# Optimization experiments

Measured on AMD Instinct MI355X. Metric: run time of the kernel, lower is better.

Reference implementation:

```python
import jax, jax.numpy as jnp
import numpy as np

N_INT4, N_INT8, K, GROUP = 6144, 2048, 8192, 128
N_TOTAL = N_INT4 + N_INT8
M = 16


def setup_inputs() -> dict:
    key = jax.random.key(0)
    ks = jax.random.split(key, 8)
    x = jax.random.normal(ks[0], (M, K), jnp.float32)
    # uint4 weights: values 0..15 (stored int32)
    w_int4 = jax.random.randint(ks[1], (N_INT4, K), 0, 16, jnp.int32)
    # group-wise scales [N_int4, K//group_size]
    s_int4 = jax.random.uniform(ks[2], (N_INT4, K // GROUP), jnp.float32, minval=0.005, maxval=0.02)
    # int8 weights stored in offset-128 form (w_int8 + 128 -> 0..255), as pack_for_marlin builds
    w_uint8 = jax.random.randint(ks[3], (N_INT8, K), 0, 256, jnp.int32)
    # per-channel int8 scales
    s_int8 = jax.random.uniform(ks[4], (N_INT8,), jnp.float32, minval=0.005, maxval=0.02)
    awq_scales = jax.random.uniform(ks[5], (K,), jnp.float32, minval=0.5, maxval=2.0)
    bias = jax.random.normal(ks[6], (N_TOTAL,), jnp.float32) * 0.01
    inv_perm = jax.random.permutation(ks[7], N_TOTAL).astype(jnp.int32)
    return dict(x=x, w_int4=w_int4, s_int4=s_int4, w_uint8=w_uint8, s_int8=s_int8,
                awq_scales=awq_scales, bias=bias, inv_perm=inv_perm, group_size=GROUP)


def reference(x, w_int4, s_int4, w_uint8, s_int8, awq_scales, bias, inv_perm, group_size):
    dt = x.dtype
    k = x.shape[-1]
    # AWQ input scaling (unfused path: x / awq_scales)
    x2 = x.reshape(-1, k) / awq_scales[None, :]
    sum_x = jnp.sum(x2, axis=1, keepdims=True)  # [M, 1]

    # Marlin uint4b8 dequant: (q - 8) * scale, group-wise scales for int4 rows
    s4_k = jnp.repeat(s_int4, group_size, axis=1)            # [N4, K]
    W4 = (w_int4.astype(dt) - 8.0) * s4_k                    # [N4, K]

    # int8 rows split into high/low nibbles with scales 16*s and s
    high = (w_uint8 >> 4) & 15
    low = w_uint8 & 15
    Wh = (high.astype(dt) - 8.0) * (16.0 * s_int8)[:, None]  # [N8, K]
    Wl = (low.astype(dt) - 8.0) * s_int8[:, None]            # [N8, K]

    Wc = jnp.concatenate([W4, Wh, Wl], axis=0)               # [N4+2*N8, K]
    y = x2 @ Wc.T                                            # marlin_gemm equivalent

    n4 = W4.shape[0]
    n8 = s_int8.shape[0]
    y4 = y[:, :n4]
    # int8 reconstruction: y_high + y_low + 8*s_int8*sum_x  == s_int8 * (x @ w_int8^T)
    y8 = y[:, n4:n4 + n8] + y[:, n4 + n8:] + (8.0 * s_int8)[None, :] * sum_x
    y_out = jnp.concatenate([y4, y8], axis=-1)[:, inv_perm] + bias[None, :]
    return y_out.reshape(*x.shape[:-1], n4 + n8)
```

## Files before the change

kernel.cpp:

```cpp
#include <hip/hip_runtime.h>
#include <hip/hip_bf16.h>

constexpr int K    = 8192;
constexpr int N4   = 6144;
constexpr int N8   = 2048;
constexpr int NT   = N4 + N8;
constexpr int NG   = K / 128;

typedef short  short8  __attribute__((ext_vector_type(8)));
typedef float  floatx4 __attribute__((ext_vector_type(4)));

__device__ inline short f2bf(float f) {
    __hip_bfloat16 h = __float2bfloat16(f);
    return __builtin_bit_cast(short, h);
}

__global__ void prep_kernel(const float* __restrict__ x,
                            const float* __restrict__ awq,
                            const int*   __restrict__ inv_perm,
                            short* __restrict__ x2bf,
                            int*   __restrict__ fwd) {
    const int tid  = blockIdx.x * blockDim.x + threadIdx.x;
    const int c    = tid >> 9;
    const int rem  = tid & 511;
    const int lane = rem >> 3;
    const int j    = rem & 7;
    const int m    = lane & 15;
    const int k    = c * 32 + (lane >> 4) * 8 + j;
    x2bf[tid] = f2bf(x[m * K + k] / awq[k]);
    if (tid < NT) fwd[inv_perm[tid]] = tid;
}

__device__ inline floatx4 chunk_mfma(int4 wa, int4 wb, short8 xv, float off,
                                     floatx4 cin) {
    short8 bf;
    bf[0] = f2bf((float)wa.x + off);
    bf[1] = f2bf((float)wa.y + off);
    bf[2] = f2bf((float)wa.z + off);
    bf[3] = f2bf((float)wa.w + off);
    bf[4] = f2bf((float)wb.x + off);
    bf[5] = f2bf((float)wb.y + off);
    bf[6] = f2bf((float)wb.z + off);
    bf[7] = f2bf((float)wb.w + off);
    return __builtin_amdgcn_mfma_f32_16x16x32_bf16(xv, bf, cin, 0, 0, 0);
}

__global__ __launch_bounds__(512)
void qgemv_kernel(const short* __restrict__ xf,
                  const int*   __restrict__ w4,
                  const float* __restrict__ s4,
                  const int*   __restrict__ w8,
                  const float* __restrict__ s8,
                  const int*   __restrict__ fwd,
                  const float* __restrict__ bias,
                  float* __restrict__ out) {
    __shared__ float lds[8 * 256];

    const int t    = threadIdx.x;
    const int lane = t & 63;
    const int w    = t >> 6;
    const int nb   = blockIdx.x * 16;
    const int i    = lane & 15;
    const int q    = lane >> 4;
    const int row  = nb + i;

    const bool  is4 = (nb < N4);
    const float off = is4 ? -8.f : -128.f;

    const int*   wp = (is4 ? (w4 + (size_t)row * K)
                           : (w8 + (size_t)(row - N4) * K))
                      + w * 1024 + q * 8;
    const short* xw = xf + ((size_t)w * 32) * 512 + lane * 8;
    const float* sp = s4 + (size_t)row * NG + w * 8;
    const float  s8row = is4 ? 0.f : s8[row - N4];

    floatx4 acc = {0.f, 0.f, 0.f, 0.f};

    int4   wA0, wA1, wA2, wA3, wB0, wB1, wB2, wB3;
    short8 xA0, xA1, xB0, xB1;
    float  sA, sB;

#define LOADSTAGE(S, W0, W1, W2, W3, X0, X1, SS)                     \
    do {                                                             \
        const int c_ = 2 * (S);                                      \
        W0 = *(const int4*)(wp + (size_t)c_ * 32);                   \
        W1 = *(const int4*)(wp + (size_t)c_ * 32 + 4);               \
        W2 = *(const int4*)(wp + (size_t)c_ * 32 + 32);              \
        W3 = *(const int4*)(wp + (size_t)c_ * 32 + 36);              \
        X0 = *(const short8*)(xw + (size_t)c_ * 512);                \
        X1 = *(const short8*)(xw + (size_t)c_ * 512 + 512);          \
        SS = is4 ? sp[(S) >> 1] : s8row;                             \
    } while (0)

#define COMPSTAGE(W0, W1, W2, W3, X0, X1, SS)                        \
    do {                                                             \
        floatx4 g_ = chunk_mfma(W0, W1, X0, off,                     \
                                (floatx4){0.f, 0.f, 0.f, 0.f});      \
        g_ = chunk_mfma(W2, W3, X1, off, g_);                        \
        acc[0] += (SS) * g_[0];                                      \
        acc[1] += (SS) * g_[1];                                      \
        acc[2] += (SS) * g_[2];                                      \
        acc[3] += (SS) * g_[3];                                      \
    } while (0)

    LOADSTAGE(0, wA0, wA1, wA2, wA3, xA0, xA1, sA);
    #pragma unroll 1
    for (int s = 0; s < 16; s += 2) {
        const int s1 = (s + 1 < 16) ? s + 1 : 15;
        LOADSTAGE(s1, wB0, wB1, wB2, wB3, xB0, xB1, sB);
        COMPSTAGE(wA0, wA1, wA2, wA3, xA0, xA1, sA);
        const int s2 = (s + 2 < 16) ? s + 2 : 15;
        LOADSTAGE(s2, wA0, wA1, wA2, wA3, xA0, xA1, sA);
        COMPSTAGE(wB0, wB1, wB2, wB3, xB0, xB1, sB);
    }
#undef LOADSTAGE
#undef COMPSTAGE

    #pragma unroll
    for (int r = 0; r < 4; ++r)
        lds[w * 256 + (q * 4 + r) * 16 + i] = acc[r];
    __syncthreads();

    if (t < 256) {
        float v = 0.f;
        #pragma unroll
        for (int ww = 0; ww < 8; ++ww) v += lds[ww * 256 + t];
        const int m  = t >> 4;
        const int i2 = t & 15;
        const int n  = nb + i2;
        const int d  = fwd[n];
        out[(size_t)m * NT + d] = v + bias[d];
    }
}

extern "C" void kernel_launch(void* const* d_in, const int* in_sizes, int n_in,
                              void* d_out, int out_size, void* d_ws, size_t ws_size,
                              hipStream_t stream) {
    const float* x        = (const float*)d_in[0];
    const int*   w_int4   = (const int*)  d_in[1];
    const float* s_int4   = (const float*)d_in[2];
    const int*   w_uint8  = (const int*)  d_in[3];
    const float* s_int8   = (const float*)d_in[4];
    const float* awq      = (const float*)d_in[5];
    const float* bias     = (const float*)d_in[6];
    const int*   inv_perm = (const int*)  d_in[7];

    short* x2bf = (short*)d_ws;
    int*   fwd  = (int*)((char*)d_ws + (size_t)16 * K * sizeof(short));

    prep_kernel<<<(16 * K) / 256, 256, 0, stream>>>(x, awq, inv_perm, x2bf, fwd);
    qgemv_kernel<<<NT / 16, 512, 0, stream>>>(x2bf, w_int4, s_int4,
                                              w_uint8, s_int8, fwd, bias,
                                              (float*)d_out);
}
```

Baseline: 368.1 us.

## Stream weights and activations via direct global-to-LDS loads with triple buffering

Replaces register-staged global loads with global_load_lds DMA into three rotating LDS buffers per wave, gated by vmcnt waits, so that several stages of loads stay in flight while the MFMAs run. Block size drops from 512 to 256 threads, with each wave covering twice the K range. Group scales are also prefetched into LDS with a single DMA. This adds LDS traffic and reads back from LDS, and each wave synchronises only through the vmcnt counter, which depends on the compiler not reordering other memory operations.

```diff
diff --git a/kernel.cpp b/kernel.cpp
--- a/kernel.cpp
+++ b/kernel.cpp
@@ -9,11 +9,19 @@
 
 typedef short  short8  __attribute__((ext_vector_type(8)));
 typedef float  floatx4 __attribute__((ext_vector_type(4)));
+typedef __attribute__((address_space(1))) void gas_t;
+typedef __attribute__((address_space(3))) void las_t;
 
 __device__ inline short f2bf(float f) {
     __hip_bfloat16 h = __float2bfloat16(f);
     return __builtin_bit_cast(short, h);
 }
+
+__device__ __forceinline__ void dma16(const void* g, void* l) {
+    __builtin_amdgcn_global_load_lds((gas_t*)g, (las_t*)l, 16, 0, 0);
+}
+
+#define WAIT_VM(N) __builtin_amdgcn_s_waitcnt(0x70 | (N))
 
 __global__ void prep_kernel(const float* __restrict__ x,
                             const float* __restrict__ awq,
@@ -31,8 +39,8 @@
     if (tid < NT) fwd[inv_perm[tid]] = tid;
 }
 
-__device__ inline floatx4 chunk_mfma(int4 wa, int4 wb, short8 xv, float off,
-                                     floatx4 cin) {
+__device__ __forceinline__ floatx4 chunk_mfma(int4 wa, int4 wb, short8 xv,
+                                              float off, floatx4 cin) {
     short8 bf;
     bf[0] = f2bf((float)wa.x + off);
     bf[1] = f2bf((float)wa.y + off);
@@ -45,7 +53,7 @@
     return __builtin_amdgcn_mfma_f32_16x16x32_bf16(xv, bf, cin, 0, 0, 0);
 }
 
-__global__ __launch_bounds__(512)
+__global__ __launch_bounds__(256)
 void qgemv_kernel(const short* __restrict__ xf,
                   const int*   __restrict__ w4,
                   const float* __restrict__ s4,
@@ -54,7 +62,10 @@
                   const int*   __restrict__ fwd,
                   const float* __restrict__ bias,
                   float* __restrict__ out) {
-    __shared__ float lds[8 * 256];
+    __shared__ int   wsl0[4][1024], wsl1[4][1024], wsl2[4][1024];
+    __shared__ short xsl0[4][1024], xsl1[4][1024], xsl2[4][1024];
+    __shared__ float scl[4][256];
+    __shared__ float red[4][256];
 
     const int t    = threadIdx.x;
     const int lane = t & 63;
@@ -67,64 +78,75 @@
     const bool  is4 = (nb < N4);
     const float off = is4 ? -8.f : -128.f;
 
-    const int*   wp = (is4 ? (w4 + (size_t)row * K)
-                           : (w8 + (size_t)(row - N4) * K))
-                      + w * 1024 + q * 8;
-    const short* xw = xf + ((size_t)w * 32) * 512 + lane * 8;
-    const float* sp = s4 + (size_t)row * NG + w * 8;
+    const int*   pw = (is4 ? (w4 + (size_t)row * K)
+                           : (w8 + (size_t)(row - N4) * K)) + w * 2048 + q * 8;
+    const short* px = xf + (size_t)w * 64 * 512 + lane * 8;
     const float  s8row = is4 ? 0.f : s8[row - N4];
+
+    if (is4) {
+        const float* ps = s4 + (size_t)(nb + (lane >> 2)) * NG + w * 16 + (lane & 3) * 4;
+        dma16(ps, &scl[w][0]);
+    }
+
+#define ISSUE(S, WSL, XSL)                                            \
+    do {                                                              \
+        const int*   pws = pw + (S) * 64;                             \
+        const short* pxs = px + (size_t)(2 * (S)) * 512;              \
+        dma16(pws,      &WSL[w][0]);                                  \
+        dma16(pws + 4,  &WSL[w][256]);                                \
+        dma16(pws + 32, &WSL[w][512]);                                \
+        dma16(pws + 36, &WSL[w][768]);                                \
+        dma16(pxs,       &XSL[w][0]);                                 \
+        dma16(pxs + 512, &XSL[w][512]);                               \
+    } while (0)
+
+#define BODY(S, WSL, XSL, NWAIT)                                      \
+    do {                                                              \
+        WAIT_VM(NWAIT);                                               \
+        const int*   wsrc = &WSL[w][0];                               \
+        const short* xsrc = &XSL[w][0];                               \
+        const int4   wv0 = *(const int4*)(wsrc + lane * 4);           \
+        const int4   wv1 = *(const int4*)(wsrc + 256 + lane * 4);     \
+        const int4   wv2 = *(const int4*)(wsrc + 512 + lane * 4);     \
+        const int4   wv3 = *(const int4*)(wsrc + 768 + lane * 4);     \
+        const short8 xv0 = *(const short8*)(xsrc + lane * 8);         \
+        const short8 xv1 = *(const short8*)(xsrc + 512 + lane * 8);   \
+        const float  sg  = is4 ? scl[w][i * 16 + ((S) >> 1)] : s8row; \
+        floatx4 g_ = chunk_mfma(wv0, wv1, xv0, off,                   \
+                                (floatx4){0.f, 0.f, 0.f, 0.f});       \
+        g_ = chunk_mfma(wv2, wv3, xv1, off, g_);                      \
+        acc[0] += sg * g_[0]; acc[1] += sg * g_[1];                   \
+        acc[2] += sg * g_[2]; acc[3] += sg * g_[3];                   \
+    } while (0)
 
     floatx4 acc = {0.f, 0.f, 0.f, 0.f};
 
-    int4   wA0, wA1, wA2, wA3, wB0, wB1, wB2, wB3;
-    short8 xA0, xA1, xB0, xB1;
-    float  sA, sB;
+    ISSUE(0, wsl0, xsl0);
+    ISSUE(1, wsl1, xsl1);
+    ISSUE(2, wsl2, xsl2);
 
-#define LOADSTAGE(S, W0, W1, W2, W3, X0, X1, SS)                     \
-    do {                                                             \
-        const int c_ = 2 * (S);                                      \
-        W0 = *(const int4*)(wp + (size_t)c_ * 32);                   \
-        W1 = *(const int4*)(wp + (size_t)c_ * 32 + 4);               \
-        W2 = *(const int4*)(wp + (size_t)c_ * 32 + 32);              \
-        W3 = *(const int4*)(wp + (size_t)c_ * 32 + 36);              \
-        X0 = *(const short8*)(xw + (size_t)c_ * 512);                \
-        X1 = *(const short8*)(xw + (size_t)c_ * 512 + 512);          \
-        SS = is4 ? sp[(S) >> 1] : s8row;                             \
-    } while (0)
+    #pragma unroll 1
+    for (int s = 0; s < 27; s += 3) {
+        BODY(s,     wsl0, xsl0, 12); ISSUE(s + 3, wsl0, xsl0);
+        BODY(s + 1, wsl1, xsl1, 12); ISSUE(s + 4, wsl1, xsl1);
+        BODY(s + 2, wsl2, xsl2, 12); ISSUE(s + 5, wsl2, xsl2);
+    }
+    BODY(27, wsl0, xsl0, 12); ISSUE(30, wsl0, xsl0);
+    BODY(28, wsl1, xsl1, 12); ISSUE(31, wsl1, xsl1);
+    BODY(29, wsl2, xsl2, 12);
+    BODY(30, wsl0, xsl0, 6);
+    BODY(31, wsl1, xsl1, 0);
 
-#define COMPSTAGE(W0, W1, W2, W3, X0, X1, SS)                        \
-    do {                                                             \
-        floatx4 g_ = chunk_mfma(W0, W1, X0, off,                     \
-                                (floatx4){0.f, 0.f, 0.f, 0.f});      \
-        g_ = chunk_mfma(W2, W3, X1, off, g_);                        \
-        acc[0] += (SS) * g_[0];                                      \
-        acc[1] += (SS) * g_[1];                                      \
-        acc[2] += (SS) * g_[2];                                      \
-        acc[3] += (SS) * g_[3];                                      \
-    } while (0)
-
-    LOADSTAGE(0, wA0, wA1, wA2, wA3, xA0, xA1, sA);
-    #pragma unroll 1
-    for (int s = 0; s < 16; s += 2) {
-        const int s1 = (s + 1 < 16) ? s + 1 : 15;
-        LOADSTAGE(s1, wB0, wB1, wB2, wB3, xB0, xB1, sB);
-        COMPSTAGE(wA0, wA1, wA2, wA3, xA0, xA1, sA);
-        const int s2 = (s + 2 < 16) ? s + 2 : 15;
-        LOADSTAGE(s2, wA0, wA1, wA2, wA3, xA0, xA1, sA);
-        COMPSTAGE(wB0, wB1, wB2, wB3, xB0, xB1, sB);
-    }
-#undef LOADSTAGE
-#undef COMPSTAGE
+#undef ISSUE
+#undef BODY
 
     #pragma unroll
     for (int r = 0; r < 4; ++r)
-        lds[w * 256 + (q * 4 + r) * 16 + i] = acc[r];
+        red[w][(q * 4 + r) * 16 + i] = acc[r];
     __syncthreads();
 
     if (t < 256) {
-        float v = 0.f;
-        #pragma unroll
-        for (int ww = 0; ww < 8; ++ww) v += lds[ww * 256 + t];
+        const float v = red[0][t] + red[1][t] + red[2][t] + red[3][t];
         const int m  = t >> 4;
         const int i2 = t & 15;
         const int n  = nb + i2;
@@ -149,7 +171,7 @@
     int*   fwd  = (int*)((char*)d_ws + (size_t)16 * K * sizeof(short));
 
     prep_kernel<<<(16 * K) / 256, 256, 0, stream>>>(x, awq, inv_perm, x2bf, fwd);
-    qgemv_kernel<<<NT / 16, 512, 0, stream>>>(x2bf, w_int4, s_int4,
+    qgemv_kernel<<<NT / 16, 256, 0, stream>>>(x2bf, w_int4, s_int4,
                                               w_uint8, s_int8, fwd, bias,
                                               (float*)d_out);
 }
```

Measured after the change: 339.4 us. 1.08x faster.

## Halve waves per block and deepen load pipeline to three stages

Applied to the files above, without the earlier changes.

Blocks now use 4 waves instead of 8, and each wave covers 2048 K-elements (32 stages instead of 16). The software pipeline becomes a three-buffer rotation with explicit prologue and epilogue, so more loads are in flight per wave, and the cross-wave LDS reduction shrinks to 4 partials. Launch bounds change to 256 threads with a minimum of 2 blocks per CU. The extra live registers from the third buffer set may limit occupancy, and fewer waves per block means less parallelism per output tile.

```diff
diff --git a/kernel.cpp b/kernel.cpp
--- a/kernel.cpp
+++ b/kernel.cpp
@@ -31,8 +31,8 @@
     if (tid < NT) fwd[inv_perm[tid]] = tid;
 }
 
-__device__ inline floatx4 chunk_mfma(int4 wa, int4 wb, short8 xv, float off,
-                                     floatx4 cin) {
+__device__ __forceinline__ floatx4 chunk_mfma(int4 wa, int4 wb, short8 xv,
+                                              float off, floatx4 cin) {
     short8 bf;
     bf[0] = f2bf((float)wa.x + off);
     bf[1] = f2bf((float)wa.y + off);
@@ -45,7 +45,7 @@
     return __builtin_amdgcn_mfma_f32_16x16x32_bf16(xv, bf, cin, 0, 0, 0);
 }
 
-__global__ __launch_bounds__(512)
+__global__ __launch_bounds__(256, 2)
 void qgemv_kernel(const short* __restrict__ xf,
                   const int*   __restrict__ w4,
                   const float* __restrict__ s4,
@@ -54,7 +54,7 @@
                   const int*   __restrict__ fwd,
                   const float* __restrict__ bias,
                   float* __restrict__ out) {
-    __shared__ float lds[8 * 256];
+    __shared__ float red[4][256];
 
     const int t    = threadIdx.x;
     const int lane = t & 63;
@@ -68,17 +68,16 @@
     const float off = is4 ? -8.f : -128.f;
 
     const int*   wp = (is4 ? (w4 + (size_t)row * K)
-                           : (w8 + (size_t)(row - N4) * K))
-                      + w * 1024 + q * 8;
-    const short* xw = xf + ((size_t)w * 32) * 512 + lane * 8;
-    const float* sp = s4 + (size_t)row * NG + w * 8;
+                           : (w8 + (size_t)(row - N4) * K)) + w * 2048 + q * 8;
+    const short* xw = xf + (size_t)w * 64 * 512 + lane * 8;
+    const float* sp = s4 + (size_t)row * NG + w * 16;
     const float  s8row = is4 ? 0.f : s8[row - N4];
 
     floatx4 acc = {0.f, 0.f, 0.f, 0.f};
 
-    int4   wA0, wA1, wA2, wA3, wB0, wB1, wB2, wB3;
-    short8 xA0, xA1, xB0, xB1;
-    float  sA, sB;
+    int4   wA0, wA1, wA2, wA3, wB0, wB1, wB2, wB3, wC0, wC1, wC2, wC3;
+    short8 xA0, xA1, xB0, xB1, xC0, xC1;
+    float  sA, sB, sC;
 
 #define LOADSTAGE(S, W0, W1, W2, W3, X0, X1, SS)                     \
     do {                                                             \
@@ -104,27 +103,36 @@
     } while (0)
 
     LOADSTAGE(0, wA0, wA1, wA2, wA3, xA0, xA1, sA);
+    LOADSTAGE(1, wB0, wB1, wB2, wB3, xB0, xB1, sB);
+    LOADSTAGE(2, wC0, wC1, wC2, wC3, xC0, xC1, sC);
+
     #pragma unroll 1
-    for (int s = 0; s < 16; s += 2) {
-        const int s1 = (s + 1 < 16) ? s + 1 : 15;
-        LOADSTAGE(s1, wB0, wB1, wB2, wB3, xB0, xB1, sB);
+    for (int s = 0; s < 27; s += 3) {
         COMPSTAGE(wA0, wA1, wA2, wA3, xA0, xA1, sA);
-        const int s2 = (s + 2 < 16) ? s + 2 : 15;
-        LOADSTAGE(s2, wA0, wA1, wA2, wA3, xA0, xA1, sA);
+        LOADSTAGE(s + 3, wA0, wA1, wA2, wA3, xA0, xA1, sA);
         COMPSTAGE(wB0, wB1, wB2, wB3, xB0, xB1, sB);
+        LOADSTAGE(s + 4, wB0, wB1, wB2, wB3, xB0, xB1, sB);
+        COMPSTAGE(wC0, wC1, wC2, wC3, xC0, xC1, sC);
+        LOADSTAGE(s + 5, wC0, wC1, wC2, wC3, xC0, xC1, sC);
     }
+    COMPSTAGE(wA0, wA1, wA2, wA3, xA0, xA1, sA);
+    LOADSTAGE(30, wA0, wA1, wA2, wA3, xA0, xA1, sA);
+    COMPSTAGE(wB0, wB1, wB2, wB3, xB0, xB1, sB);
+    LOADSTAGE(31, wB0, wB1, wB2, wB3, xB0, xB1, sB);
+    COMPSTAGE(wC0, wC1, wC2, wC3, xC0, xC1, sC);
+    COMPSTAGE(wA0, wA1, wA2, wA3, xA0, xA1, sA);
+    COMPSTAGE(wB0, wB1, wB2, wB3, xB0, xB1, sB);
+
 #undef LOADSTAGE
 #undef COMPSTAGE
 
     #pragma unroll
     for (int r = 0; r < 4; ++r)
-        lds[w * 256 + (q * 4 + r) * 16 + i] = acc[r];
+        red[w][(q * 4 + r) * 16 + i] = acc[r];
     __syncthreads();
 
     if (t < 256) {
-        float v = 0.f;
-        #pragma unroll
-        for (int ww = 0; ww < 8; ++ww) v += lds[ww * 256 + t];
+        const float v = red[0][t] + red[1][t] + red[2][t] + red[3][t];
         const int m  = t >> 4;
         const int i2 = t & 15;
         const int n  = nb + i2;
@@ -149,7 +157,7 @@
     int*   fwd  = (int*)((char*)d_ws + (size_t)16 * K * sizeof(short));
 
     prep_kernel<<<(16 * K) / 256, 256, 0, stream>>>(x, awq, inv_perm, x2bf, fwd);
-    qgemv_kernel<<<NT / 16, 512, 0, stream>>>(x2bf, w_int4, s_int4,
+    qgemv_kernel<<<NT / 16, 256, 0, stream>>>(x2bf, w_int4, s_int4,
                                               w_uint8, s_int8, fwd, bias,
                                               (float*)d_out);
 }
```

After: 344.5 us. 6.4% less time.
